# Performance work log

Measured on AMD Instinct MI355X. Metric: run time of the kernel, lower is better.

The kernel has to match this reference:

```python
import jax, jax.numpy as jnp
import numpy as np

SCALE = 64.0
BASE_MARGIN = 0.3
EPS = 1e-12  # torch F.normalize eps

B, D, C, K = 512, 512, 50000, 3


def _l2norm(x, axis):
    n = jnp.sqrt(jnp.sum(x * x, axis=axis, keepdims=True))
    return x / jnp.maximum(n, EPS)


def setup_inputs() -> dict:
    key = jax.random.key(0)
    k1, k2, k3 = jax.random.split(key, 3)
    input = jax.random.normal(k1, (B, D), dtype=jnp.float32)
    label = jax.random.randint(k2, (B,), 0, C, dtype=jnp.int64)
    # xavier-uniform-ish init for weights
    limit = float(np.sqrt(6.0 / (C * K + D)))
    weights = jax.random.uniform(k3, (C * K, D), dtype=jnp.float32, minval=-limit, maxval=limit)
    margins = jnp.ones((C,), dtype=jnp.float32) * BASE_MARGIN
    return {"input": input, "label": label, "weights": weights, "margins": margins}


def reference(input, label, weights, margins):
    batch = input.shape[0]
    num_classes = margins.shape[0]
    k = weights.shape[0] // num_classes

    x = _l2norm(input, axis=1)          # (B, D)
    w = _l2norm(weights, axis=1)        # (C*K, D)
    # cosine similarities: (B, C, K)
    cos = jnp.einsum("bd,nd->bn", x, w).reshape(batch, num_classes, k)
    max_cos = jnp.max(cos, axis=2)      # (B, C)

    bidx = jnp.arange(batch)
    target_cos = max_cos[bidx, label]               # (B,)
    cls_cos = cos[bidx, label]                      # (B, K): sub-center cosines of true class
    # avg angular shift between main center and sub-centers
    avg_shift = jnp.sum(jnp.abs(cls_cos[:, :1] - cls_cos[:, 1:]), axis=1) / (k - 1)
    weighted_margin = margins[label] * (1.0 + avg_shift)
    max_cos = max_cos.at[bidx, label].set(target_cos - weighted_margin)
    return SCALE * max_cos
```

## Files before the change

kernel.cpp:

```cpp
#include <hip/hip_runtime.h>
#include <hip/hip_bf16.h>
#include <stdint.h>

#define BATCH   512
#define DIMS    512
#define NCLS    50000
#define KSUB    3
#define NW      150000
#define SCALE_F 64.0f
#define EPS_F   1e-12f

typedef __bf16 bf16x8 __attribute__((ext_vector_type(8)));
typedef __bf16 bf16x4 __attribute__((ext_vector_type(4)));
typedef float  f32x4  __attribute__((ext_vector_type(4)));

__device__ __forceinline__ void gld16(const void* g, void* l) {
  __builtin_amdgcn_global_load_lds((const __attribute__((address_space(1))) void*)g,
                                   (__attribute__((address_space(3))) void*)l, 16, 0, 0);
}

__global__ __launch_bounds__(256) void normalize_all(
    const float* __restrict__ w, const float* __restrict__ x,
    __bf16* __restrict__ wb, __bf16* __restrict__ xb) {
  int wave = threadIdx.x >> 6, lane = threadIdx.x & 63;
  int r = blockIdx.x * 4 + wave;
  if (r >= NW + BATCH) return;
  const float* src;
  __bf16* dst;
  if (r < NW) { src = w + (size_t)r * DIMS; dst = wb + (size_t)r * DIMS; }
  else        { int r2 = r - NW; src = x + (size_t)r2 * DIMS; dst = xb + (size_t)r2 * DIMS; }

  const float4* rp = (const float4*)src;
  float4 v0 = rp[lane];
  float4 v1 = rp[lane + 64];
  float s = v0.x*v0.x + v0.y*v0.y + v0.z*v0.z + v0.w*v0.w
          + v1.x*v1.x + v1.y*v1.y + v1.z*v1.z + v1.w*v1.w;
  #pragma unroll
  for (int m = 1; m < 64; m <<= 1) s += __shfl_xor(s, m, 64);
  float inv = 1.0f / fmaxf(sqrtf(s), EPS_F);

  bf16x4 o0, o1;
  o0[0] = (__bf16)(v0.x * inv); o0[1] = (__bf16)(v0.y * inv);
  o0[2] = (__bf16)(v0.z * inv); o0[3] = (__bf16)(v0.w * inv);
  o1[0] = (__bf16)(v1.x * inv); o1[1] = (__bf16)(v1.y * inv);
  o1[2] = (__bf16)(v1.z * inv); o1[3] = (__bf16)(v1.w * inv);
  bf16x4* wp = (bf16x4*)dst;
  wp[lane]      = o0;
  wp[lane + 64] = o1;
}

#define BM 128
#define BN 192
#define BK 64
#define BUFB 40960
#define NTILE 8
#define NCT  782

__global__ __launch_bounds__(256, 2) void gemm_max3(
    const __bf16* __restrict__ xb, const __bf16* __restrict__ wb,
    float* __restrict__ out) {
  __shared__ __align__(16) char smem[2 * BUFB];

  const int bx   = blockIdx.x;
  const int xcd  = bx & 7;
  const int ci   = bx >> 3;
  const int mt   = ci & 3;
  const int ct   = (ci >> 2) * 8 + xcd;
  if (ct >= NCT) return;

  const int tid  = threadIdx.x;
  const int wave = tid >> 6;
  const int lane = tid & 63;
  const int m0   = mt * BM;
  const int n0   = ct * BN;

  const int wm   = wave & 1;
  const int wn   = wave >> 1;
  const int l15  = lane & 15;
  const int quad = lane >> 4;

  const int srow = lane >> 3;
  const int scol = (((lane & 7) ^ srow) << 3);

  f32x4 acc[4][6] = {};

  auto stage = [&](int kk, char* buf) {
    unsigned short* As = (unsigned short*)buf;
    unsigned short* Bs = (unsigned short*)(buf + 16384);
    #pragma unroll
    for (int s10 = 0; s10 < 10; ++s10) {
      int s = wave * 10 + s10;
      if (s < 16) {
        int row = s * 8 + srow;
        gld16(xb + (size_t)(m0 + row) * DIMS + kk + scol, As + s * 512);
      } else {
        int t = s - 16;
        int grow = n0 + t * 8 + srow;
        if (grow > NW - 1) grow = NW - 1;
        gld16(wb + (size_t)grow * DIMS + kk + scol, Bs + t * 512);
      }
    }
  };

  auto compute = [&](const char* buf) {
    const unsigned short* As = (const unsigned short*)buf;
    const unsigned short* Bs = (const unsigned short*)(buf + 16384);
    #pragma unroll
    for (int h = 0; h < 2; ++h) {
      bf16x8 a[4], bfr[6];
      #pragma unroll
      for (int i = 0; i < 4; ++i) {
        int r = wm * 64 + i * 16 + l15;
        int slot = (h * 4 + quad) ^ (r & 7);
        a[i] = *(const bf16x8*)(As + r * 64 + slot * 8);
      }
      #pragma unroll
      for (int j = 0; j < 6; ++j) {
        int r = wn * 96 + j * 16 + l15;
        int slot = (h * 4 + quad) ^ (r & 7);
        bfr[j] = *(const bf16x8*)(Bs + r * 64 + slot * 8);
      }
      #pragma unroll
      for (int i = 0; i < 4; ++i)
        #pragma unroll
        for (int j = 0; j < 6; ++j)
          acc[i][j] = __builtin_amdgcn_mfma_f32_16x16x32_bf16(a[i], bfr[j], acc[i][j], 0, 0, 0);
    }
  };

  stage(0, smem);
  __syncthreads();

  int p = 0;
  #pragma unroll 1
  for (int kk = BK; kk < DIMS; kk += BK) {
    stage(kk, smem + (p ^ 1) * BUFB);
    compute(smem + p * BUFB);
    __syncthreads();
    p ^= 1;
  }
  compute(smem + p * BUFB);
  __syncthreads();

  float* scr = (float*)smem + wave * 1600;
  const int rl   = lane >> 2;
  const int gblk = lane & 3;
  #pragma unroll
  for (int i = 0; i < 4; ++i) {
    #pragma unroll
    for (int j = 0; j < 6; ++j)
      #pragma unroll
      for (int r = 0; r < 4; ++r)
        scr[(quad * 4 + r) * 100 + j * 16 + l15] = acc[i][j][r] * SCALE_F;
    __asm__ volatile("s_waitcnt lgkmcnt(0)" ::: "memory");

    float f[24];
    const float4* srcp = (const float4*)(scr + rl * 100 + gblk * 24);
    #pragma unroll
    for (int t = 0; t < 6; ++t) *(float4*)(f + 4 * t) = srcp[t];

    float o[8];
    #pragma unroll
    for (int t = 0; t < 8; ++t)
      o[t] = fmaxf(f[3 * t], fmaxf(f[3 * t + 1], f[3 * t + 2]));

    int brow = m0 + wm * 64 + i * 16 + rl;
    int cls0 = ct * 64 + wn * 32 + gblk * 8;
    float* op = out + (size_t)brow * NCLS + cls0;
    if (cls0 + 8 <= NCLS) {
      float4 s0 = {o[0], o[1], o[2], o[3]};
      float4 s1 = {o[4], o[5], o[6], o[7]};
      *(float4*)op = s0;
      *(float4*)(op + 4) = s1;
    } else {
      #pragma unroll
      for (int t = 0; t < 8; ++t)
        if (cls0 + t < NCLS) op[t] = o[t];
    }
    __asm__ volatile("s_waitcnt lgkmcnt(0)" ::: "memory");
  }
}

__device__ __forceinline__ float d4(float4 a, float4 b) {
  return a.x * b.x + a.y * b.y + a.z * b.z + a.w * b.w;
}

__global__ __launch_bounds__(64) void fix_labels(
    const float* __restrict__ x, const int* __restrict__ label,
    const float* __restrict__ w, const float* __restrict__ margins,
    float* __restrict__ out) {
  int b = blockIdx.x;
  int lane = threadIdx.x;
  int c = label[b];
  const float4* xr = (const float4*)(x + (size_t)b * DIMS);
  const float4* w0 = (const float4*)(w + (size_t)(3 * c + 0) * DIMS);
  const float4* w1 = (const float4*)(w + (size_t)(3 * c + 1) * DIMS);
  const float4* w2 = (const float4*)(w + (size_t)(3 * c + 2) * DIMS);

  float xx = 0, n0 = 0, n1 = 0, n2 = 0, p0 = 0, p1 = 0, p2 = 0;
  #pragma unroll
  for (int t = 0; t < 2; ++t) {
    int i = lane + t * 64;
    float4 xv = xr[i], a0 = w0[i], a1 = w1[i], a2 = w2[i];
    xx += d4(xv, xv);
    n0 += d4(a0, a0); n1 += d4(a1, a1); n2 += d4(a2, a2);
    p0 += d4(xv, a0); p1 += d4(xv, a1); p2 += d4(xv, a2);
  }
  #pragma unroll
  for (int m = 1; m < 64; m <<= 1) {
    xx += __shfl_xor(xx, m, 64);
    n0 += __shfl_xor(n0, m, 64); n1 += __shfl_xor(n1, m, 64); n2 += __shfl_xor(n2, m, 64);
    p0 += __shfl_xor(p0, m, 64); p1 += __shfl_xor(p1, m, 64); p2 += __shfl_xor(p2, m, 64);
  }
  if (lane == 0) {
    float rx = 1.0f / fmaxf(sqrtf(xx), EPS_F);
    float r0 = 1.0f / fmaxf(sqrtf(n0), EPS_F);
    float r1 = 1.0f / fmaxf(sqrtf(n1), EPS_F);
    float r2 = 1.0f / fmaxf(sqrtf(n2), EPS_F);
    float c0 = p0 * rx * r0, c1 = p1 * rx * r1, c2 = p2 * rx * r2;
    float tgt = fmaxf(c0, fmaxf(c1, c2));
    float shift = 0.5f * (fabsf(c0 - c1) + fabsf(c0 - c2));
    float wm = margins[c] * (1.0f + shift);
    out[(size_t)b * NCLS + c] = SCALE_F * (tgt - wm);
  }
}

extern "C" void kernel_launch(void* const* d_in, const int* in_sizes, int n_in,
                              void* d_out, int out_size, void* d_ws, size_t ws_size,
                              hipStream_t stream) {
  const float* input   = (const float*)d_in[0];
  const int*   label   = (const int*)d_in[1];
  const float* weights = (const float*)d_in[2];
  const float* margins = (const float*)d_in[3];
  float* out = (float*)d_out;

  __bf16* w_bf = (__bf16*)d_ws;
  __bf16* x_bf = w_bf + (size_t)NW * DIMS;

  normalize_all<<<(NW + BATCH) / 4, 256, 0, stream>>>(weights, input, w_bf, x_bf);
  gemm_max3<<<3136, 256, 0, stream>>>(x_bf, w_bf, out);
  fix_labels<<<BATCH, 64, 0, stream>>>(input, label, weights, margins, out);
}
```

Before: 551.7 us.

## Fuse weight normalization and bf16 conversion into GEMM B-tile loading

Drops the separate pass that normalized all 150000 weight rows to bf16 in workspace. The GEMM now loads raw fp32 weights into registers, converts them to bf16 into swizzled LDS, and accumulates per-row sums of squares. The inverse norm is applied to the accumulators in the epilogue. This removes a full read plus bf16 write of the weight matrix, but the GEMM now reads fp32 weights once per M-tile (4 times), adds register pressure, and converts in the loop.

```diff
diff --git a/kernel.cpp b/kernel.cpp
--- a/kernel.cpp
+++ b/kernel.cpp
@@ -19,16 +19,13 @@
                                    (__attribute__((address_space(3))) void*)l, 16, 0, 0);
 }
 
-__global__ __launch_bounds__(256) void normalize_all(
-    const float* __restrict__ w, const float* __restrict__ x,
-    __bf16* __restrict__ wb, __bf16* __restrict__ xb) {
+__global__ __launch_bounds__(256) void normalize_x(
+    const float* __restrict__ x, __bf16* __restrict__ xb) {
   int wave = threadIdx.x >> 6, lane = threadIdx.x & 63;
   int r = blockIdx.x * 4 + wave;
-  if (r >= NW + BATCH) return;
-  const float* src;
-  __bf16* dst;
-  if (r < NW) { src = w + (size_t)r * DIMS; dst = wb + (size_t)r * DIMS; }
-  else        { int r2 = r - NW; src = x + (size_t)r2 * DIMS; dst = xb + (size_t)r2 * DIMS; }
+  if (r >= BATCH) return;
+  const float* src = x + (size_t)r * DIMS;
+  __bf16* dst = xb + (size_t)r * DIMS;
 
   const float4* rp = (const float4*)src;
   float4 v0 = rp[lane];
@@ -53,11 +50,10 @@
 #define BN 192
 #define BK 64
 #define BUFB 40960
-#define NTILE 8
 #define NCT  782
 
 __global__ __launch_bounds__(256, 2) void gemm_max3(
-    const __bf16* __restrict__ xb, const __bf16* __restrict__ wb,
+    const __bf16* __restrict__ xb, const float* __restrict__ wf,
     float* __restrict__ out) {
   __shared__ __align__(16) char smem[2 * BUFB];
 
@@ -83,22 +79,38 @@
   const int scol = (((lane & 7) ^ srow) << 3);
 
   f32x4 acc[4][6] = {};
-
-  auto stage = [&](int kk, char* buf) {
+  float bsq[12] = {};
+  float4 bv[12];
+
+  auto bload = [&](int kk) {
+    #pragma unroll
+    for (int s12 = 0; s12 < 12; ++s12) {
+      int row  = s12 * 16 + (tid >> 4);
+      int c4   = lane & 15;
+      int grow = n0 + row; if (grow > NW - 1) grow = NW - 1;
+      bv[s12] = *((const float4*)(wf + (size_t)grow * DIMS + kk) + c4);
+    }
+  };
+  auto bstore = [&](char* buf) {
+    unsigned short* Bs = (unsigned short*)(buf + 16384);
+    #pragma unroll
+    for (int s12 = 0; s12 < 12; ++s12) {
+      int row = s12 * 16 + (tid >> 4);
+      int c4  = lane & 15;
+      float4 v = bv[s12];
+      bsq[s12] += v.x*v.x + v.y*v.y + v.z*v.z + v.w*v.w;
+      bf16x4 o;
+      o[0] = (__bf16)v.x; o[1] = (__bf16)v.y; o[2] = (__bf16)v.z; o[3] = (__bf16)v.w;
+      int slot = (c4 >> 1) ^ (row & 7);
+      *(bf16x4*)(Bs + row * 64 + slot * 8 + (c4 & 1) * 4) = o;
+    }
+  };
+  auto aload = [&](int kk, char* buf) {
     unsigned short* As = (unsigned short*)buf;
-    unsigned short* Bs = (unsigned short*)(buf + 16384);
-    #pragma unroll
-    for (int s10 = 0; s10 < 10; ++s10) {
-      int s = wave * 10 + s10;
-      if (s < 16) {
-        int row = s * 8 + srow;
-        gld16(xb + (size_t)(m0 + row) * DIMS + kk + scol, As + s * 512);
-      } else {
-        int t = s - 16;
-        int grow = n0 + t * 8 + srow;
-        if (grow > NW - 1) grow = NW - 1;
-        gld16(wb + (size_t)grow * DIMS + kk + scol, Bs + t * 512);
-      }
+    #pragma unroll
+    for (int s4 = 0; s4 < 4; ++s4) {
+      int s = wave * 4 + s4;
+      gld16(xb + (size_t)(m0 + s * 8 + srow) * DIMS + kk + scol, As + s * 512);
     }
   };
 
@@ -128,19 +140,35 @@
     }
   };
 
-  stage(0, smem);
+  bload(0); aload(0, smem); bstore(smem);
   __syncthreads();
 
   int p = 0;
   #pragma unroll 1
   for (int kk = BK; kk < DIMS; kk += BK) {
-    stage(kk, smem + (p ^ 1) * BUFB);
+    bload(kk);
+    aload(kk, smem + (p ^ 1) * BUFB);
     compute(smem + p * BUFB);
+    bstore(smem + (p ^ 1) * BUFB);
     __syncthreads();
     p ^= 1;
   }
   compute(smem + p * BUFB);
   __syncthreads();
+
+  float* sqlds = (float*)(smem + 26624);
+  #pragma unroll
+  for (int k = 0; k < 12; ++k) {
+    float v = bsq[k];
+    v += __shfl_xor(v, 1, 64); v += __shfl_xor(v, 2, 64);
+    v += __shfl_xor(v, 4, 64); v += __shfl_xor(v, 8, 64);
+    if ((lane & 15) == 0) sqlds[16 * k + wave * 4 + (lane >> 4)] = v;
+  }
+  __syncthreads();
+  float invw6[6];
+  #pragma unroll
+  for (int j = 0; j < 6; ++j)
+    invw6[j] = 1.0f / fmaxf(sqrtf(sqlds[wn * 96 + j * 16 + l15]), EPS_F);
 
   float* scr = (float*)smem + wave * 1600;
   const int rl   = lane >> 2;
@@ -151,7 +179,7 @@
     for (int j = 0; j < 6; ++j)
       #pragma unroll
       for (int r = 0; r < 4; ++r)
-        scr[(quad * 4 + r) * 100 + j * 16 + l15] = acc[i][j][r] * SCALE_F;
+        scr[(quad * 4 + r) * 100 + j * 16 + l15] = acc[i][j][r] * SCALE_F * invw6[j];
     __asm__ volatile("s_waitcnt lgkmcnt(0)" ::: "memory");
 
     float f[24];
@@ -234,10 +262,9 @@
   const float* margins = (const float*)d_in[3];
   float* out = (float*)d_out;
 
-  __bf16* w_bf = (__bf16*)d_ws;
-  __bf16* x_bf = w_bf + (size_t)NW * DIMS;
-
-  normalize_all<<<(NW + BATCH) / 4, 256, 0, stream>>>(weights, input, w_bf, x_bf);
-  gemm_max3<<<3136, 256, 0, stream>>>(x_bf, w_bf, out);
+  __bf16* x_bf = (__bf16*)d_ws;
+
+  normalize_x<<<BATCH / 4, 256, 0, stream>>>(input, x_bf);
+  gemm_max3<<<3136, 256, 0, stream>>>(x_bf, weights, out);
   fix_labels<<<BATCH, 64, 0, stream>>>(input, label, weights, margins, out);
 }
```

Measured after the change: 541.2 us. No clear change (-1.9%).
